# Optimization experiments

Measured on AMD Instinct MI355X. Metric: run time of the kernel, lower is better.

Reference implementation:

```python
import jax, jax.numpy as jnp
import numpy as np

D_MODEL = 1024
NUM_HEAD = 16
D_HEAD = 64
SEQ = 1024
MEM = 1024
BATCH = 4
LN_EPS = 1e-5


def _rel_shift(x):
    # x: [i, j, b, n] -- Transformer-XL relative shift trick
    i, j, b, n = x.shape
    zero_pad = jnp.zeros((i, 1, b, n), dtype=x.dtype)
    x_padded = jnp.concatenate([zero_pad, x], axis=1).reshape(j + 1, i, b, n)
    return x_padded[1:].reshape(i, j, b, n)


def setup_inputs() -> dict:
    key = jax.random.key(0)
    ks = jax.random.split(key, 8)
    w_scale = 1.0 / np.sqrt(D_MODEL)  # keep activations O(1)
    total = MEM + SEQ
    return {
        "x": jax.random.normal(ks[0], (SEQ, BATCH, D_MODEL), jnp.float32),
        "memory": jax.random.normal(ks[1], (MEM, BATCH, D_MODEL), jnp.float32),
        "pos_emb": jax.random.normal(ks[2], (total, BATCH, D_MODEL), jnp.float32),
        "pos_bias_u": jax.random.normal(ks[3], (NUM_HEAD, D_HEAD), jnp.float32) * 0.02,
        "pos_bias_v": jax.random.normal(ks[4], (NUM_HEAD, D_HEAD), jnp.float32) * 0.02,
        "W_qkv": jax.random.normal(ks[5], (3 * NUM_HEAD * D_HEAD, D_MODEL), jnp.float32) * w_scale,
        "W_rel": jax.random.normal(ks[6], (NUM_HEAD * D_HEAD, D_MODEL), jnp.float32) * w_scale,
        "W_o": jax.random.normal(ks[7], (D_MODEL, NUM_HEAD * D_HEAD), jnp.float32) * w_scale,
        "ln_gamma": jnp.ones((D_MODEL,), jnp.float32),
        "ln_beta": jnp.zeros((D_MODEL,), jnp.float32),
    }


def reference(x, memory, pos_emb, pos_bias_u, pos_bias_v, W_qkv, W_rel, W_o, ln_gamma, ln_beta):
    seq_len = x.shape[0]
    c = jnp.concatenate([memory, x], axis=0)        # [T, B, D]
    T, B = c.shape[0], c.shape[1]
    n, d = pos_bias_u.shape
    scale = 1.0 / np.sqrt(d)

    heads = c @ W_qkv.T                              # [T, B, 3*n*d]
    q, k, v = jnp.split(heads, 3, axis=-1)
    q = q.reshape(T, B, n, d)[-seq_len:]             # [S, B, n, d]
    k = k.reshape(T, B, n, d)                        # [T, B, n, d]
    v = v.reshape(T, B, n, d)
    r = (pos_emb @ W_rel.T).reshape(T, B, n, d)      # [T, B, n, d]

    AC = jnp.einsum('ibnd,jbnd->ijbn', q + pos_bias_u, k)
    BD = _rel_shift(jnp.einsum('ibnd,jbnd->ijbn', q + pos_bias_v, r))
    attn_score = (AC + BD) * scale                   # [S, T, B, n]
    attn_prob = jax.nn.softmax(attn_score, axis=1)   # softmax over key dim (dropout = eval identity)

    attn_vec = jnp.einsum('ijbn,jbnd->ibnd', attn_prob, v).reshape(seq_len, B, n * d)
    attn_out = attn_vec @ W_o.T                      # [S, B, D]

    y = x + attn_out
    mu = jnp.mean(y, axis=-1, keepdims=True)
    var = jnp.mean(jnp.square(y - mu), axis=-1, keepdims=True)
    return ln_gamma * (y - mu) / jnp.sqrt(var + LN_EPS) + ln_beta
```

## Files before the change

kernel.cpp:

```cpp
#include <hip/hip_runtime.h>

#define S_ 1024
#define M_ 1024
#define T_ 2048
#define B_ 4
#define H_ 16
#define DM_ 1024
#define DH_ 64

typedef __attribute__((ext_vector_type(8))) short s16x8;
typedef __attribute__((ext_vector_type(16))) float f32x16;

__device__ __forceinline__ unsigned short f2b(float x){
  unsigned int u = __float_as_uint(x);
  u = (u + 0x7fffu + ((u>>16)&1u)) >> 16;
  return (unsigned short)u;
}
__device__ __forceinline__ float b2f(unsigned short h){
  return __uint_as_float(((unsigned int)h)<<16);
}
__device__ __forceinline__ uint4 pack8(const float* v){
  uint4 o;
  o.x = (unsigned)f2b(v[0]) | ((unsigned)f2b(v[1])<<16);
  o.y = (unsigned)f2b(v[2]) | ((unsigned)f2b(v[3])<<16);
  o.z = (unsigned)f2b(v[4]) | ((unsigned)f2b(v[5])<<16);
  o.w = (unsigned)f2b(v[6]) | ((unsigned)f2b(v[7])<<16);
  return o;
}
__device__ __forceinline__ void glds16(const unsigned short* g, unsigned short* l){
  __builtin_amdgcn_global_load_lds((const __attribute__((address_space(1))) void*)g,
                                   (__attribute__((address_space(3))) void*)l, 16, 0, 0);
}

#define BAR_L()   asm volatile("s_waitcnt lgkmcnt(0)\ns_barrier" ::: "memory")
#define BAR_VL()  asm volatile("s_waitcnt vmcnt(0) lgkmcnt(0)\ns_barrier" ::: "memory")
#define BAR_V6L() asm volatile("s_waitcnt vmcnt(6) lgkmcnt(0)\ns_barrier" ::: "memory")

__global__ __launch_bounds__(256) void cast_all(
    const float* __restrict__ mem, const float* __restrict__ x,
    const float* __restrict__ pos, const float* __restrict__ wqkv,
    const float* __restrict__ wrel, const float* __restrict__ wo,
    unsigned short* __restrict__ c16, unsigned short* __restrict__ pos16,
    unsigned short* __restrict__ wq16, unsigned short* __restrict__ wr16,
    unsigned short* __restrict__ wo16)
{
  int u = blockIdx.x*256 + threadIdx.x;
  const float* s; unsigned short* d;
  if (u < 1048576)      { s = (u < 524288) ? mem + (size_t)u*8 : x + (size_t)(u-524288)*8;
                          d = c16 + (size_t)u*8; }
  else if (u < 2097152) { int v = u - 1048576; s = pos  + (size_t)v*8; d = pos16 + (size_t)v*8; }
  else if (u < 2490368) { int v = u - 2097152; s = wqkv + (size_t)v*8; d = wq16  + (size_t)v*8; }
  else if (u < 2621440) { int v = u - 2490368; s = wrel + (size_t)v*8; d = wr16  + (size_t)v*8; }
  else                  { int v = u - 2621440; s = wo   + (size_t)v*8; d = wo16  + (size_t)v*8; }
  float4 x0 = *(const float4*)s;
  float4 x1 = *(const float4*)(s+4);
  float f[8] = {x0.x,x0.y,x0.z,x0.w,x1.x,x1.y,x1.z,x1.w};
  *(uint4*)d = pack8(f);
}

__global__ __launch_bounds__(256) void gemm_nt(const unsigned short* __restrict__ A,
    const unsigned short* __restrict__ Bw, void* __restrict__ Cout,
    const float* __restrict__ res, int Ntot, int K, int mode)
{
  __shared__ __align__(16) unsigned short a_s[128*64];
  __shared__ __align__(16) unsigned short b_s[128*64];
  const int tid = threadIdx.x;
  const int lane = tid & 63, wave = tid >> 6;
  const int wr = wave >> 1, wc = wave & 1;
  const long m0 = (long)blockIdx.y * 128, n0 = (long)blockIdx.x * 128;
  f32x16 acc[2][2];
  for (int qa=0;qa<2;qa++) for(int qb=0;qb<2;qb++) for (int e=0;e<16;e++) acc[qa][qb][e]=0.f;
  int srow[4], scol[4];
  for (int c = 0; c < 4; c++) {
    int ch = c*256 + tid;
    srow[c] = ch >> 3;
    scol[c] = (((ch & 7) ^ (srow[c] & 7))) * 8;
  }
  for (int k0 = 0; k0 < K; k0 += 64) {
    for (int c = 0; c < 4; c++) {
      int ch = c*256 + tid;
      glds16(&A[(size_t)(m0+srow[c])*K + k0 + scol[c]], &a_s[ch*8]);
      glds16(&Bw[(size_t)(n0+srow[c])*K + k0 + scol[c]], &b_s[ch*8]);
    }
    __syncthreads();
    for (int ks = 0; ks < 4; ks++) {
      const int kb = ks*2 + (lane>>5);
      s16x8 af[2], bf[2];
      for (int q = 0; q < 2; q++) {
        int ra = wr*64 + q*32 + (lane&31);
        int rb = wc*64 + q*32 + (lane&31);
        af[q] = *(const s16x8*)&a_s[ra*64 + ((kb ^ (ra&7))<<3)];
        bf[q] = *(const s16x8*)&b_s[rb*64 + ((kb ^ (rb&7))<<3)];
      }
      for (int qr=0;qr<2;qr++)
        for (int qc2=0;qc2<2;qc2++)
          acc[qr][qc2] = __builtin_amdgcn_mfma_f32_32x32x16_bf16(af[qr], bf[qc2], acc[qr][qc2], 0,0,0);
    }
    __syncthreads();
  }
  for (int qr=0;qr<2;qr++)
    for (int qc2=0;qc2<2;qc2++)
      for (int e=0;e<16;e++){
        long row = m0 + wr*64 + qr*32 + (e&3) + 8*(e>>2) + 4*(lane>>5);
        long col = n0 + wc*64 + qc2*32 + (lane&31);
        size_t o = (size_t)row*Ntot + col;
        if (mode == 0) ((unsigned short*)Cout)[o] = f2b(acc[qr][qc2][e]);
        else           ((float*)Cout)[o] = acc[qr][qc2][e] + res[o];
      }
}

__global__ __launch_bounds__(256) void gemm4(
    const unsigned short* __restrict__ c16, const unsigned short* __restrict__ pos16,
    const unsigned short* __restrict__ wq16, const unsigned short* __restrict__ wr16,
    const float* __restrict__ u, const float* __restrict__ v,
    unsigned short* __restrict__ Kb, unsigned short* __restrict__ relo,
    unsigned short* __restrict__ QU, unsigned short* __restrict__ QV,
    unsigned short* __restrict__ VT)
{
  __shared__ __align__(16) unsigned short a_s[128*64];
  __shared__ __align__(16) unsigned short b_s[128*64];
  const int tid = threadIdx.x;
  const int lane = tid & 63, wave = tid >> 6;
  const int wr = wave >> 1, wc = wave & 1;

  const int id = blockIdx.x;
  int role, bx, by, bz = 0;
  if      (id < 512)  { role = 0; bx = id & 7;  by = id >> 3; }
  else if (id < 1024) { role = 1; int t = id - 512;  bx = t & 7;  by = t >> 3; }
  else if (id < 1280) { role = 2; int t = id - 1024; bx = t & 7;  by = t >> 3; }
  else                { role = 3; int t = id - 1280; bx = t & 15; by = (t >> 4) & 7; bz = t >> 7; }
  const long m0 = (long)by * 128, n0 = (long)bx * 128;

  const unsigned short* A  = (role==0) ? c16 :
                             (role==1) ? pos16 :
                             (role==2) ? c16 + (size_t)4096*1024 :
                                         wq16 + (size_t)2048*1024;
  const unsigned short* Bw = (role==0) ? wq16 + (size_t)1024*1024 :
                             (role==1) ? wr16 :
                             (role==2) ? wq16 : c16;

  f32x16 acc[2][2];
  for (int qa=0;qa<2;qa++) for(int qb=0;qb<2;qb++) for (int e=0;e<16;e++) acc[qa][qb][e]=0.f;

  size_t aOff[4], bOff[4];
  for (int c = 0; c < 4; c++) {
    int ch = c*256 + tid;
    int srow = ch >> 3;
    int scol = ((ch & 7) ^ (srow & 7)) * 8;
    aOff[c] = (size_t)(m0+srow)*1024 + scol;
    bOff[c] = (role==3) ? (((size_t)(n0+srow)*4 + bz)*1024 + scol)
                        : ((size_t)(n0+srow)*1024 + scol);
  }

  for (int k0 = 0; k0 < 1024; k0 += 64) {
    for (int c = 0; c < 4; c++) {
      int ch = c*256 + tid;
      glds16(&A [aOff[c] + k0], &a_s[ch*8]);
      glds16(&Bw[bOff[c] + k0], &b_s[ch*8]);
    }
    __syncthreads();
    for (int ks = 0; ks < 4; ks++) {
      const int kb = ks*2 + (lane>>5);
      s16x8 af[2], bf[2];
      for (int q = 0; q < 2; q++) {
        int ra = wr*64 + q*32 + (lane&31);
        int rb = wc*64 + q*32 + (lane&31);
        af[q] = *(const s16x8*)&a_s[ra*64 + ((kb ^ (ra&7))<<3)];
        bf[q] = *(const s16x8*)&b_s[rb*64 + ((kb ^ (rb&7))<<3)];
      }
      for (int qr=0;qr<2;qr++)
        for (int qc2=0;qc2<2;qc2++)
          acc[qr][qc2] = __builtin_amdgcn_mfma_f32_32x32x16_bf16(af[qr], bf[qc2], acc[qr][qc2], 0,0,0);
    }
    __syncthreads();
  }

  for (int qr=0;qr<2;qr++)
    for (int qc2=0;qc2<2;qc2++)
      for (int e=0;e<16;e++){
        long row = m0 + wr*64 + qr*32 + (e&3) + 8*(e>>2) + 4*(lane>>5);
        long col = n0 + wc*64 + qc2*32 + (lane&31);
        float a = acc[qr][qc2][e];
        if (role == 0)      Kb  [(size_t)row*1024 + col] = f2b(a);
        else if (role == 1) relo[(size_t)row*1024 + col] = f2b(a);
        else if (role == 2) {
          size_t dst = (((size_t)(row&3)*16 + (col>>6))*1024 + (row>>2))*64 + (col&63);
          QU[dst] = f2b(a + u[col]);
          QV[dst] = f2b(a + v[col]);
        } else {
          VT[(size_t)bz*2097152 + (size_t)row*2048 + col] = f2b(a);
        }
      }
}

__global__ __launch_bounds__(256,2) void flash_attn4(
    const unsigned short* __restrict__ QU, const unsigned short* __restrict__ QV,
    const unsigned short* __restrict__ Kb, const unsigned short* __restrict__ VT,
    const unsigned short* __restrict__ relo, unsigned short* __restrict__ AV)
{
  __shared__ __align__(16) unsigned short qv_s[65*72];
  __shared__ __align__(16) unsigned short k_s [2][64*64];
  __shared__ __align__(16) unsigned short vt_s[64*64];
  __shared__ __align__(16) unsigned short rg_s[2][128*64];
  __shared__ __align__(16) unsigned short p_s [64*64];
  __shared__ float l_s[64];

  const int tid = threadIdx.x, lane = tid&63, wave = tid>>6;
  const int bh = blockIdx.x, b = bh>>4, h = bh&15;
  const int i0 = blockIdx.y*64;
  const int qr = wave>>1, qc = wave&1;
  const int hi = lane>>5, ll = lane&31;
  const unsigned short* QUb = QU + (size_t)bh*S_*DH_;
  const unsigned short* QVb = QV + (size_t)bh*S_*DH_;
  const unsigned short* Kg  = Kb + (size_t)b*1024 + h*64;
  const unsigned short* VTb = VT + (size_t)bh*64*T_;
  const unsigned short* Rg  = relo + (size_t)b*1024 + h*64;

  const int s0r = tid>>3,        s0c = (((tid&7)       ^ (s0r&7)))*8;
  const int s1r = (256+tid)>>3,  s1c = ((((256+tid)&7) ^ (s1r&7)))*8;

  glds16(&Kg [(size_t)(0+s0r)*4096 + s0c], &k_s[0][(size_t)tid*8]);
  glds16(&Kg [(size_t)(0+s1r)*4096 + s1c], &k_s[0][(size_t)(256+tid)*8]);
  {
    const int wb0 = 0 - i0 + 960;
    for (int c=0;c<4;c++){
      int ch = c*256+tid; int rr = ch>>3, off = ch&7;
      int t = wb0 + rr; t = t < 0 ? 0 : (t > T_-1 ? T_-1 : t);
      glds16(&Rg[(size_t)t*4096 + ((off ^ (rr&7)))*8], &rg_s[0][(size_t)ch*8]);
    }
  }
  for (int c=0;c<2;c++){
    int ch = c*256+tid; int row = ch>>3, off=(ch&7);
    *(uint4*)&p_s[row*64 + ((off ^ (row&7))<<3)] = *(const uint4*)&QUb[(size_t)(i0+row)*64 + off*8];
    *(uint4*)&qv_s[row*72+off*8] = *(const uint4*)&QVb[(size_t)(i0+row)*64 + off*8];
  }
  if (tid < 8) {
    int rr = i0 + 64; if (rr > S_-1) rr = S_-1;
    *(uint4*)&qv_s[64*72 + tid*8] = *(const uint4*)&QVb[(size_t)rr*64 + tid*8];
  }
  BAR_L();

  s16x8 qur0, qur1, qur2, qur3;
  s16x8 qv00, qv01, qv02, qv03;
  {
    const int rq = qr*32 + ll;
    qur0 = *(const s16x8*)&p_s[rq*64 + (((0*2+hi) ^ (rq&7))<<3)];
    qur1 = *(const s16x8*)&p_s[rq*64 + (((1*2+hi) ^ (rq&7))<<3)];
    qur2 = *(const s16x8*)&p_s[rq*64 + (((2*2+hi) ^ (rq&7))<<3)];
    qur3 = *(const s16x8*)&p_s[rq*64 + (((3*2+hi) ^ (rq&7))<<3)];
    const int ro = rq*72 + hi*8;
    qv00 = *(const s16x8*)&qv_s[ro +  0];
    qv01 = *(const s16x8*)&qv_s[ro + 16];
    qv02 = *(const s16x8*)&qv_s[ro + 32];
    qv03 = *(const s16x8*)&qv_s[ro + 48];
  }

  s16x8 ones;
  for (int e=0;e<8;e++) ones[e] = (short)0x3F80;

  f32x16 acc_o, acc_l;
  for (int e=0;e<16;e++){ acc_o[e]=0.f; acc_l[e]=0.f; }

  const int col = qc*32 + ll;
  const int cbase = (qc - qr + 1) * 32;

  int cur = 0;
  for (int j0 = 0; j0 < T_; j0 += 64) {
    const int jdmax = j0 + 63 - i0;
    const int jdmin = j0 - 63 - i0;
    const int cls = (jdmax <= 1024) ? 0 : ((jdmin >= 1026) ? 2 : 1);
    const int jn = j0 + 64;
    unsigned short* kc = &k_s[cur][0];
    unsigned short* rc = &rg_s[cur][0];
    unsigned short* kn = &k_s[cur^1][0];
    unsigned short* rn = &rg_s[cur^1][0];

    BAR_VL();

    glds16(&VTb[(size_t)s0r*T_ + j0 + s0c], &vt_s[(size_t)tid*8]);
    glds16(&VTb[(size_t)s1r*T_ + j0 + s1c], &vt_s[(size_t)(256+tid)*8]);
    if (jn < T_) {
      glds16(&Kg[(size_t)(jn+s0r)*4096 + s0c], &kn[(size_t)tid*8]);
      glds16(&Kg[(size_t)(jn+s1r)*4096 + s1c], &kn[(size_t)(256+tid)*8]);
      const int jdmaxn = jn + 63 - i0;
      const int jdminn = jn - 63 - i0;
      const int clsn = (jdmaxn <= 1024) ? 0 : ((jdminn >= 1026) ? 2 : 1);
      const int wbn = (clsn == 2) ? (jn - i0 - 1089) : (jn - i0 + 960);
      for (int c=0;c<4;c++){
        int ch = c*256+tid; int rr = ch>>3, off = ch&7;
        int t = wbn + rr; t = t < 0 ? 0 : (t > T_-1 ? T_-1 : t);
        glds16(&Rg[(size_t)t*4096 + ((off ^ (rr&7)))*8], &rn[(size_t)ch*8]);
      }
    }

    s16x8 av0, av1, av2, av3;
    if (cls == 2) {
      const int ro1 = (qr*32+ll+1)*72 + hi*8;
      av0 = *(const s16x8*)&qv_s[ro1 +  0];
      av1 = *(const s16x8*)&qv_s[ro1 + 16];
      av2 = *(const s16x8*)&qv_s[ro1 + 32];
      av3 = *(const s16x8*)&qv_s[ro1 + 48];
    } else {
      av0 = qv00; av1 = qv01; av2 = qv02; av3 = qv03;
    }

    f32x16 gacc0, gacc1;
    for (int e=0;e<16;e++){ gacc0[e]=0.f; gacc1[e]=0.f; }
    __builtin_amdgcn_s_setprio(1);
#define BANDK(KS, AV) { \
      int kb = KS*2 + hi; \
      { int br = cbase + ll; \
        s16x8 bb = *(const s16x8*)&rc[br*64 + ((kb ^ (br&7))<<3)]; \
        gacc0 = __builtin_amdgcn_mfma_f32_32x32x16_bf16(AV, bb, gacc0, 0,0,0); } \
      { int br = cbase + 32 + ll; \
        s16x8 bb = *(const s16x8*)&rc[br*64 + ((kb ^ (br&7))<<3)]; \
        gacc1 = __builtin_amdgcn_mfma_f32_32x32x16_bf16(AV, bb, gacc1, 0,0,0); } }
    BANDK(0, av0) BANDK(1, av1) BANDK(2, av2) BANDK(3, av3)

    f32x16 acc;
    for (int e=0;e<16;e++) acc[e]=0.f;
#define ACK(KS, AU) { \
      int kb = KS*2 + hi; \
      int rbk = qc*32 + ll; \
      s16x8 bq = *(const s16x8*)&kc[rbk*64 + ((kb ^ (rbk&7))<<3)]; \
      acc = __builtin_amdgcn_mfma_f32_32x32x16_bf16(AU, bq, acc, 0,0,0); }
    ACK(0, qur0) ACK(1, qur1) ACK(2, qur2) ACK(3, qur3)
    __builtin_amdgcn_s_setprio(0);

    for (int e=0;e<16;e++){
      int rm = 4*hi + (e&3) + 8*(e>>2);
      int r  = qr*32 + rm;
      int jd = j0 + col - (i0 + r);
      int tl = (ll + rm + 1) & 31;
      float sel = (tl > rm) ? gacc1[e] : gacc0[e];
      int li = ((((ll - rm + 31) & 31) | (hi<<5)) << 2);
      float bd = __uint_as_float((unsigned)__builtin_amdgcn_ds_bpermute(li, (int)__float_as_uint(sel)));
      if (jd == 1025) bd = 0.f;
      float p = __expf((acc[e] + bd) * 0.125f);
      if (!(cls == 1 && jd >= 1026))
        p_s[r*64 + (((col>>3) ^ (r&7))<<3) + (col&7)] = f2b(p);
    }

    if (cls == 1) {
      BAR_L();
      const int wb2 = j0 - i0 - 1089;
      for (int c=0;c<4;c++){
        int ch = c*256+tid; int rr = ch>>3, off = ch&7;
        int t = wb2 + rr; t = t < 0 ? 0 : (t > T_-1 ? T_-1 : t);
        glds16(&Rg[(size_t)t*4096 + ((off ^ (rr&7)))*8], &rc[(size_t)ch*8]);
      }
      BAR_VL();
      f32x16 g2a, g2b;
      for (int e=0;e<16;e++){ g2a[e]=0.f; g2b[e]=0.f; }
      __builtin_amdgcn_s_setprio(1);
#define BANDW(KS) { \
        int kb = KS*2 + hi; \
        const int ro1 = (qr*32+ll+1)*72 + hi*8; \
        s16x8 a = *(const s16x8*)&qv_s[ro1 + KS*16]; \
        { int br = cbase + ll; \
          s16x8 bb = *(const s16x8*)&rc[br*64 + ((kb ^ (br&7))<<3)]; \
          g2a = __builtin_amdgcn_mfma_f32_32x32x16_bf16(a, bb, g2a, 0,0,0); } \
        { int br = cbase + 32 + ll; \
          s16x8 bb = *(const s16x8*)&rc[br*64 + ((kb ^ (br&7))<<3)]; \
          g2b = __builtin_amdgcn_mfma_f32_32x32x16_bf16(a, bb, g2b, 0,0,0); } }
      BANDW(0) BANDW(1) BANDW(2) BANDW(3)
      __builtin_amdgcn_s_setprio(0);
      for (int e=0;e<16;e++){
        int rm = 4*hi + (e&3) + 8*(e>>2);
        int r  = qr*32 + rm;
        int jd = j0 + col - (i0 + r);
        int tl = (ll + rm + 1) & 31;
        float sel = (tl > rm) ? g2b[e] : g2a[e];
        int li = ((((ll - rm + 31) & 31) | (hi<<5)) << 2);
        float bd = __uint_as_float((unsigned)__builtin_amdgcn_ds_bpermute(li, (int)__float_as_uint(sel)));
        float p = __expf((acc[e] + bd) * 0.125f);
        if (jd >= 1026)
          p_s[r*64 + (((col>>3) ^ (r&7))<<3) + (col&7)] = f2b(p);
      }
    }

    if (jn < T_) { BAR_V6L(); } else { BAR_VL(); }

    __builtin_amdgcn_s_setprio(1);
    for (int ks=0; ks<4; ks++){
      int kb = ks*2 + hi;
      int rv = qr*32 + ll, rbv = qc*32 + ll;
      s16x8 a  = *(const s16x8*)&p_s[rv*64 + ((kb ^ (rv&7))<<3)];
      s16x8 bv = *(const s16x8*)&vt_s[rbv*64 + ((kb ^ (rbv&7))<<3)];
      acc_o = __builtin_amdgcn_mfma_f32_32x32x16_bf16(a, bv, acc_o, 0,0,0);
      acc_l = __builtin_amdgcn_mfma_f32_32x32x16_bf16(a, ones, acc_l, 0,0,0);
    }
    __builtin_amdgcn_s_setprio(0);
    cur ^= 1;
  }

  if (qc == 0 && ll == 0) {
    for (int e=0;e<16;e++){
      int r = qr*32 + 4*hi + (e&3) + 8*(e>>2);
      l_s[r] = acc_l[e];
    }
  }
  BAR_L();
  for (int e=0;e<16;e++){
    int r = qr*32 + 4*hi + (e&3) + 8*(e>>2);
    float oo = acc_o[e] / l_s[r];
    AV[ ((size_t)(i0+r)*B_ + b)*(H_*DH_) + h*DH_ + col ] = f2b(oo);
  }
#undef BANDK
#undef ACK
#undef BANDW
}

__global__ __launch_bounds__(256) void ln_kernel(const float* __restrict__ y,
    const float* __restrict__ g, const float* __restrict__ be, float* __restrict__ o)
{
  __shared__ float red[8];
  int row = blockIdx.x, tid = threadIdx.x;
  const float* yr = y + (size_t)row*DM_;
  float v[4];
  for (int e=0;e<4;e++) v[e] = yr[tid + 256*e];
  float s = v[0]+v[1]+v[2]+v[3];
  for (int off=32; off>0; off>>=1) s += __shfl_down(s, off, 64);
  if ((tid&63)==0) red[tid>>6] = s;
  __syncthreads();
  if (tid==0) red[4] = red[0]+red[1]+red[2]+red[3];
  __syncthreads();
  float mu = red[4] * (1.f/DM_);
  __syncthreads();
  float q = 0.f;
  for (int e=0;e<4;e++){ float d = v[e]-mu; q += d*d; }
  for (int off=32; off>0; off>>=1) q += __shfl_down(q, off, 64);
  if ((tid&63)==0) red[tid>>6] = q;
  __syncthreads();
  if (tid==0) red[4] = red[0]+red[1]+red[2]+red[3];
  __syncthreads();
  float rstd = rsqrtf(red[4]*(1.f/DM_) + 1e-5f);
  for (int e=0;e<4;e++){
    int c = tid + 256*e;
    o[(size_t)row*DM_ + c] = g[c]*(v[e]-mu)*rstd + be[c];
  }
}

extern "C" void kernel_launch(void* const* d_in, const int* in_sizes, int n_in,
                              void* d_out, int out_size, void* d_ws, size_t ws_size,
                              hipStream_t stream)
{
  const float* x    = (const float*)d_in[0];
  const float* mem  = (const float*)d_in[1];
  const float* pos  = (const float*)d_in[2];
  const float* pbu  = (const float*)d_in[3];
  const float* pbv  = (const float*)d_in[4];
  const float* wqkv = (const float*)d_in[5];
  const float* wrel = (const float*)d_in[6];
  const float* wo   = (const float*)d_in[7];
  const float* gam  = (const float*)d_in[8];
  const float* bet  = (const float*)d_in[9];
  float* out = (float*)d_out;

  char* w = (char*)d_ws;
  unsigned short* Kb    = (unsigned short*)(w + 0);
  unsigned short* relo  = (unsigned short*)(w + 16777216);
  unsigned short* wo16  = (unsigned short*)(w + 33554432);
  unsigned short* QUb   = (unsigned short*)(w + 35651584);
  unsigned short* QVb   = (unsigned short*)(w + 44040192);
  unsigned short* VT    = (unsigned short*)(w + 52428800);
  unsigned short* av16  = (unsigned short*)(w + 69206016);
  float*          yf    = (float*)(w + 77594624);
  unsigned short* c16   = (unsigned short*)(w + 94371840);
  unsigned short* pos16 = (unsigned short*)(w + 111149056);
  unsigned short* wq16  = (unsigned short*)(w + 127926272);
  unsigned short* wr16  = (unsigned short*)(w + 134217728);

  cast_all<<<10752, 256, 0, stream>>>(mem, x, pos, wqkv, wrel, wo,
                                      c16, pos16, wq16, wr16, wo16);

  gemm4<<<1792, 256, 0, stream>>>(c16, pos16, wq16, wr16, pbu, pbv,
                                  Kb, relo, QUb, QVb, VT);

  flash_attn4<<<dim3(64,16), 256, 0, stream>>>(QUb, QVb, Kb, VT, relo, av16);

  gemm_nt<<<dim3(8,32), 256, 0, stream>>>(av16, wo16, (void*)yf, x, 1024, 1024, 1);
  ln_kernel<<<4096, 256, 0, stream>>>(yf, gam, bet, out);
}
```

Measured before the change: 439.5 us.

## Load K, rel-pos and V fragments directly into registers, dropping LDS staging

The attention kernel no longer stages K, relative-position and V^T tiles through double-buffered shared memory. Each wave now loads its own MFMA B-operand fragments straight from global memory into registers, with the next tile prefetched in software while the current one is computed. This removes LDS traffic, LDS capacity use and the vmcnt barriers. In exchange, different waves re-read the same data from global memory through cache, register pressure grows (48+ extra VGPRs) and the 16-byte loads are strided across rows, so coalescing suffers.

```diff
diff --git a/kernel.cpp b/kernel.cpp
--- a/kernel.cpp
+++ b/kernel.cpp
@@ -33,8 +33,6 @@
 }
 
 #define BAR_L()   asm volatile("s_waitcnt lgkmcnt(0)\ns_barrier" ::: "memory")
-#define BAR_VL()  asm volatile("s_waitcnt vmcnt(0) lgkmcnt(0)\ns_barrier" ::: "memory")
-#define BAR_V6L() asm volatile("s_waitcnt vmcnt(6) lgkmcnt(0)\ns_barrier" ::: "memory")
 
 __global__ __launch_bounds__(256) void cast_all(
     const float* __restrict__ mem, const float* __restrict__ x,
@@ -199,9 +197,6 @@
     const unsigned short* __restrict__ relo, unsigned short* __restrict__ AV)
 {
   __shared__ __align__(16) unsigned short qv_s[65*72];
-  __shared__ __align__(16) unsigned short k_s [2][64*64];
-  __shared__ __align__(16) unsigned short vt_s[64*64];
-  __shared__ __align__(16) unsigned short rg_s[2][128*64];
   __shared__ __align__(16) unsigned short p_s [64*64];
   __shared__ float l_s[64];
 
@@ -216,19 +211,34 @@
   const unsigned short* VTb = VT + (size_t)bh*64*T_;
   const unsigned short* Rg  = relo + (size_t)b*1024 + h*64;
 
-  const int s0r = tid>>3,        s0c = (((tid&7)       ^ (s0r&7)))*8;
-  const int s1r = (256+tid)>>3,  s1c = ((((256+tid)&7) ^ (s1r&7)))*8;
-
-  glds16(&Kg [(size_t)(0+s0r)*4096 + s0c], &k_s[0][(size_t)tid*8]);
-  glds16(&Kg [(size_t)(0+s1r)*4096 + s1c], &k_s[0][(size_t)(256+tid)*8]);
-  {
-    const int wb0 = 0 - i0 + 960;
-    for (int c=0;c<4;c++){
-      int ch = c*256+tid; int rr = ch>>3, off = ch&7;
-      int t = wb0 + rr; t = t < 0 ? 0 : (t > T_-1 ? T_-1 : t);
-      glds16(&Rg[(size_t)t*4096 + ((off ^ (rr&7)))*8], &rg_s[0][(size_t)ch*8]);
-    }
-  }
+  const int col = qc*32 + ll;
+  const int cbase = (qc - qr + 1) * 32;
+  const int rbk = qc*32 + ll;
+  const int br0 = cbase + ll, br1 = cbase + 32 + ll;
+
+  uint4 rK0,rK1,rK2,rK3;
+  uint4 rR00,rR01,rR02,rR03;
+  uint4 rR10,rR11,rR12,rR13;
+  uint4 rV0,rV1,rV2,rV3;
+
+#define LOADK(J) { const unsigned short* pk_ = Kg + (size_t)((J)+rbk)*4096 + hi*8; \
+    rK0 = *(const uint4*)(pk_);    rK1 = *(const uint4*)(pk_+16); \
+    rK2 = *(const uint4*)(pk_+32); rK3 = *(const uint4*)(pk_+48); }
+#define LOADR(J, CLS) { \
+    int wb_ = ((CLS)==2) ? ((J)-i0-1089) : ((J)-i0+960); \
+    int t0_ = wb_+br0; t0_ = t0_<0?0:(t0_>T_-1?T_-1:t0_); \
+    int t1_ = wb_+br1; t1_ = t1_<0?0:(t1_>T_-1?T_-1:t1_); \
+    const unsigned short* p0_ = Rg + (size_t)t0_*4096 + hi*8; \
+    const unsigned short* p1_ = Rg + (size_t)t1_*4096 + hi*8; \
+    rR00 = *(const uint4*)(p0_);    rR01 = *(const uint4*)(p0_+16); \
+    rR02 = *(const uint4*)(p0_+32); rR03 = *(const uint4*)(p0_+48); \
+    rR10 = *(const uint4*)(p1_);    rR11 = *(const uint4*)(p1_+16); \
+    rR12 = *(const uint4*)(p1_+32); rR13 = *(const uint4*)(p1_+48); }
+#define LOADV(J) { const unsigned short* pv_ = VTb + (size_t)rbk*2048 + (J) + hi*8; \
+    rV0 = *(const uint4*)(pv_);    rV1 = *(const uint4*)(pv_+16); \
+    rV2 = *(const uint4*)(pv_+32); rV3 = *(const uint4*)(pv_+48); }
+
+  LOADK(0); LOADR(0, 0); LOADV(0);
   for (int c=0;c<2;c++){
     int ch = c*256+tid; int row = ch>>3, off=(ch&7);
     *(uint4*)&p_s[row*64 + ((off ^ (row&7))<<3)] = *(const uint4*)&QUb[(size_t)(i0+row)*64 + off*8];
@@ -261,37 +271,13 @@
   f32x16 acc_o, acc_l;
   for (int e=0;e<16;e++){ acc_o[e]=0.f; acc_l[e]=0.f; }
 
-  const int col = qc*32 + ll;
-  const int cbase = (qc - qr + 1) * 32;
-
-  int cur = 0;
   for (int j0 = 0; j0 < T_; j0 += 64) {
     const int jdmax = j0 + 63 - i0;
     const int jdmin = j0 - 63 - i0;
     const int cls = (jdmax <= 1024) ? 0 : ((jdmin >= 1026) ? 2 : 1);
     const int jn = j0 + 64;
-    unsigned short* kc = &k_s[cur][0];
-    unsigned short* rc = &rg_s[cur][0];
-    unsigned short* kn = &k_s[cur^1][0];
-    unsigned short* rn = &rg_s[cur^1][0];
-
-    BAR_VL();
-
-    glds16(&VTb[(size_t)s0r*T_ + j0 + s0c], &vt_s[(size_t)tid*8]);
-    glds16(&VTb[(size_t)s1r*T_ + j0 + s1c], &vt_s[(size_t)(256+tid)*8]);
-    if (jn < T_) {
-      glds16(&Kg[(size_t)(jn+s0r)*4096 + s0c], &kn[(size_t)tid*8]);
-      glds16(&Kg[(size_t)(jn+s1r)*4096 + s1c], &kn[(size_t)(256+tid)*8]);
-      const int jdmaxn = jn + 63 - i0;
-      const int jdminn = jn - 63 - i0;
-      const int clsn = (jdmaxn <= 1024) ? 0 : ((jdminn >= 1026) ? 2 : 1);
-      const int wbn = (clsn == 2) ? (jn - i0 - 1089) : (jn - i0 + 960);
-      for (int c=0;c<4;c++){
-        int ch = c*256+tid; int rr = ch>>3, off = ch&7;
-        int t = wbn + rr; t = t < 0 ? 0 : (t > T_-1 ? T_-1 : t);
-        glds16(&Rg[(size_t)t*4096 + ((off ^ (rr&7)))*8], &rn[(size_t)ch*8]);
-      }
-    }
+
+    BAR_L();
 
     s16x8 av0, av1, av2, av3;
     if (cls == 2) {
@@ -307,25 +293,30 @@
     f32x16 gacc0, gacc1;
     for (int e=0;e<16;e++){ gacc0[e]=0.f; gacc1[e]=0.f; }
     __builtin_amdgcn_s_setprio(1);
-#define BANDK(KS, AV) { \
-      int kb = KS*2 + hi; \
-      { int br = cbase + ll; \
-        s16x8 bb = *(const s16x8*)&rc[br*64 + ((kb ^ (br&7))<<3)]; \
-        gacc0 = __builtin_amdgcn_mfma_f32_32x32x16_bf16(AV, bb, gacc0, 0,0,0); } \
-      { int br = cbase + 32 + ll; \
-        s16x8 bb = *(const s16x8*)&rc[br*64 + ((kb ^ (br&7))<<3)]; \
-        gacc1 = __builtin_amdgcn_mfma_f32_32x32x16_bf16(AV, bb, gacc1, 0,0,0); } }
-    BANDK(0, av0) BANDK(1, av1) BANDK(2, av2) BANDK(3, av3)
+    gacc0 = __builtin_amdgcn_mfma_f32_32x32x16_bf16(av0, *(const s16x8*)&rR00, gacc0, 0,0,0);
+    gacc1 = __builtin_amdgcn_mfma_f32_32x32x16_bf16(av0, *(const s16x8*)&rR10, gacc1, 0,0,0);
+    gacc0 = __builtin_amdgcn_mfma_f32_32x32x16_bf16(av1, *(const s16x8*)&rR01, gacc0, 0,0,0);
+    gacc1 = __builtin_amdgcn_mfma_f32_32x32x16_bf16(av1, *(const s16x8*)&rR11, gacc1, 0,0,0);
+    gacc0 = __builtin_amdgcn_mfma_f32_32x32x16_bf16(av2, *(const s16x8*)&rR02, gacc0, 0,0,0);
+    gacc1 = __builtin_amdgcn_mfma_f32_32x32x16_bf16(av2, *(const s16x8*)&rR12, gacc1, 0,0,0);
+    gacc0 = __builtin_amdgcn_mfma_f32_32x32x16_bf16(av3, *(const s16x8*)&rR03, gacc0, 0,0,0);
+    gacc1 = __builtin_amdgcn_mfma_f32_32x32x16_bf16(av3, *(const s16x8*)&rR13, gacc1, 0,0,0);
 
     f32x16 acc;
     for (int e=0;e<16;e++) acc[e]=0.f;
-#define ACK(KS, AU) { \
-      int kb = KS*2 + hi; \
-      int rbk = qc*32 + ll; \
-      s16x8 bq = *(const s16x8*)&kc[rbk*64 + ((kb ^ (rbk&7))<<3)]; \
-      acc = __builtin_amdgcn_mfma_f32_32x32x16_bf16(AU, bq, acc, 0,0,0); }
-    ACK(0, qur0) ACK(1, qur1) ACK(2, qur2) ACK(3, qur3)
+    acc = __builtin_amdgcn_mfma_f32_32x32x16_bf16(qur0, *(const s16x8*)&rK0, acc, 0,0,0);
+    acc = __builtin_amdgcn_mfma_f32_32x32x16_bf16(qur1, *(const s16x8*)&rK1, acc, 0,0,0);
+    acc = __builtin_amdgcn_mfma_f32_32x32x16_bf16(qur2, *(const s16x8*)&rK2, acc, 0,0,0);
+    acc = __builtin_amdgcn_mfma_f32_32x32x16_bf16(qur3, *(const s16x8*)&rK3, acc, 0,0,0);
     __builtin_amdgcn_s_setprio(0);
+
+    if (jn < T_) {
+      const int jdmaxn = jn + 63 - i0;
+      const int jdminn = jn - 63 - i0;
+      const int clsn = (jdmaxn <= 1024) ? 0 : ((jdminn >= 1026) ? 2 : 1);
+      LOADK(jn);
+      LOADR(jn, clsn);
+    }
 
     for (int e=0;e<16;e++){
       int rm = 4*hi + (e&3) + 8*(e>>2);
@@ -342,28 +333,34 @@
     }
 
     if (cls == 1) {
-      BAR_L();
-      const int wb2 = j0 - i0 - 1089;
-      for (int c=0;c<4;c++){
-        int ch = c*256+tid; int rr = ch>>3, off = ch&7;
-        int t = wb2 + rr; t = t < 0 ? 0 : (t > T_-1 ? T_-1 : t);
-        glds16(&Rg[(size_t)t*4096 + ((off ^ (rr&7)))*8], &rc[(size_t)ch*8]);
-      }
-      BAR_VL();
+      uint4 rW00,rW01,rW02,rW03, rW10,rW11,rW12,rW13;
+      {
+        const int wb2 = j0 - i0 - 1089;
+        int t0_ = wb2+br0; t0_ = t0_<0?0:(t0_>T_-1?T_-1:t0_);
+        int t1_ = wb2+br1; t1_ = t1_<0?0:(t1_>T_-1?T_-1:t1_);
+        const unsigned short* p0_ = Rg + (size_t)t0_*4096 + hi*8;
+        const unsigned short* p1_ = Rg + (size_t)t1_*4096 + hi*8;
+        rW00 = *(const uint4*)(p0_);    rW01 = *(const uint4*)(p0_+16);
+        rW02 = *(const uint4*)(p0_+32); rW03 = *(const uint4*)(p0_+48);
+        rW10 = *(const uint4*)(p1_);    rW11 = *(const uint4*)(p1_+16);
+        rW12 = *(const uint4*)(p1_+32); rW13 = *(const uint4*)(p1_+48);
+      }
+      const int ro1 = (qr*32+ll+1)*72 + hi*8;
+      s16x8 aw0 = *(const s16x8*)&qv_s[ro1 +  0];
+      s16x8 aw1 = *(const s16x8*)&qv_s[ro1 + 16];
+      s16x8 aw2 = *(const s16x8*)&qv_s[ro1 + 32];
+      s16x8 aw3 = *(const s16x8*)&qv_s[ro1 + 48];
       f32x16 g2a, g2b;
       for (int e=0;e<16;e++){ g2a[e]=0.f; g2b[e]=0.f; }
       __builtin_amdgcn_s_setprio(1);
-#define BANDW(KS) { \
-        int kb = KS*2 + hi; \
-        const int ro1 = (qr*32+ll+1)*72 + hi*8; \
-        s16x8 a = *(const s16x8*)&qv_s[ro1 + KS*16]; \
-        { int br = cbase + ll; \
-          s16x8 bb = *(const s16x8*)&rc[br*64 + ((kb ^ (br&7))<<3)]; \
-          g2a = __builtin_amdgcn_mfma_f32_32x32x16_bf16(a, bb, g2a, 0,0,0); } \
-        { int br = cbase + 32 + ll; \
-          s16x8 bb = *(const s16x8*)&rc[br*64 + ((kb ^ (br&7))<<3)]; \
-          g2b = __builtin_amdgcn_mfma_f32_32x32x16_bf16(a, bb, g2b, 0,0,0); } }
-      BANDW(0) BANDW(1) BANDW(2) BANDW(3)
+      g2a = __builtin_amdgcn_mfma_f32_32x32x16_bf16(aw0, *(const s16x8*)&rW00, g2a, 0,0,0);
+      g2b = __builtin_amdgcn_mfma_f32_32x32x16_bf16(aw0, *(const s16x8*)&rW10, g2b, 0,0,0);
+      g2a = __builtin_amdgcn_mfma_f32_32x32x16_bf16(aw1, *(const s16x8*)&rW01, g2a, 0,0,0);
+      g2b = __builtin_amdgcn_mfma_f32_32x32x16_bf16(aw1, *(const s16x8*)&rW11, g2b, 0,0,0);
+      g2a = __builtin_amdgcn_mfma_f32_32x32x16_bf16(aw2, *(const s16x8*)&rW02, g2a, 0,0,0);
+      g2b = __builtin_amdgcn_mfma_f32_32x32x16_bf16(aw2, *(const s16x8*)&rW12, g2b, 0,0,0);
+      g2a = __builtin_amdgcn_mfma_f32_32x32x16_bf16(aw3, *(const s16x8*)&rW03, g2a, 0,0,0);
+      g2b = __builtin_amdgcn_mfma_f32_32x32x16_bf16(aw3, *(const s16x8*)&rW13, g2b, 0,0,0);
       __builtin_amdgcn_s_setprio(0);
       for (int e=0;e<16;e++){
         int rm = 4*hi + (e&3) + 8*(e>>2);
@@ -379,19 +376,22 @@
       }
     }
 
-    if (jn < T_) { BAR_V6L(); } else { BAR_VL(); }
+    BAR_L();
 
     __builtin_amdgcn_s_setprio(1);
     for (int ks=0; ks<4; ks++){
       int kb = ks*2 + hi;
-      int rv = qr*32 + ll, rbv = qc*32 + ll;
-      s16x8 a  = *(const s16x8*)&p_s[rv*64 + ((kb ^ (rv&7))<<3)];
-      s16x8 bv = *(const s16x8*)&vt_s[rbv*64 + ((kb ^ (rbv&7))<<3)];
+      int rv = qr*32 + ll;
+      s16x8 a = *(const s16x8*)&p_s[rv*64 + ((kb ^ (rv&7))<<3)];
+      s16x8 bv = (ks==0) ? *(const s16x8*)&rV0 :
+                 (ks==1) ? *(const s16x8*)&rV1 :
+                 (ks==2) ? *(const s16x8*)&rV2 : *(const s16x8*)&rV3;
       acc_o = __builtin_amdgcn_mfma_f32_32x32x16_bf16(a, bv, acc_o, 0,0,0);
       acc_l = __builtin_amdgcn_mfma_f32_32x32x16_bf16(a, ones, acc_l, 0,0,0);
     }
     __builtin_amdgcn_s_setprio(0);
-    cur ^= 1;
+
+    if (jn < T_) LOADV(jn);
   }
 
   if (qc == 0 && ll == 0) {
@@ -406,9 +406,9 @@
     float oo = acc_o[e] / l_s[r];
     AV[ ((size_t)(i0+r)*B_ + b)*(H_*DH_) + h*DH_ + col ] = f2b(oo);
   }
-#undef BANDK
-#undef ACK
-#undef BANDW
+#undef LOADK
+#undef LOADR
+#undef LOADV
 }
 
 __global__ __launch_bounds__(256) void ln_kernel(const float* __restrict__ y,
```

Measured after the change: 643.7 us. +46.5%, slower.
